# Optimization experiments

Measured on AMD Instinct MI355X. Metric: run time of the kernel, lower is better.

Reference implementation:

```python
import jax, jax.numpy as jnp
import numpy as np

B = 256      # batch
ZD = 128     # z_dim
HIN = 128    # H_inputs
H = 512      # hidden
HT = 32      # H_t
N = 16384    # num nodes
RW = 16      # rw_len
TEMP = 1.0
P_DROP = 0.2
EPS_C = 0.1  # constraints epsilon


def setup_inputs() -> dict:
    key = jax.random.key(0)
    ks = jax.random.split(key, 20)
    def w(k, shape, fan):
        return (jax.random.normal(k, shape, jnp.float32) / np.float32(np.sqrt(fan)))
    z = lambda n: jnp.zeros((n,), jnp.float32)
    u = jax.random.uniform(ks[14], (RW, B, N), jnp.float32)
    return {
        "latent": jax.random.normal(ks[0], (B, ZD + 1), jnp.float32),
        "inputs0": jnp.zeros((B, HIN), jnp.float32),
        "Wc": w(ks[1], (ZD, ZD + 1), ZD + 1), "bc": z(ZD),
        "Ws": w(ks[2], (H, ZD), ZD), "bs": z(H),
        "Wh": w(ks[3], (H, H), H), "bh": z(H),
        "Wcc": w(ks[4], (H, H), H), "bcc": z(H),
        "W_ih": w(ks[5], (4 * H, HIN), HIN), "b_ih": z(4 * H),
        "W_hh": w(ks[6], (4 * H, H), H), "b_hh": z(4 * H),
        "W_up": w(ks[7], (N, H), H), "b_up": z(N),
        "W_down": w(ks[8], (HIN, N), N),
        "Wt_down": w(ks[9], (HT, H), H), "bt_down": z(HT),
        "Wt_pred": w(ks[10], (1, HT), HT),
        "Wt_up": w(ks[11], (HT, 1), 1), "bt_up": z(HT),
        "W_vt": w(ks[12], (HIN, HIN + HT), HIN + HT),
        "W_prob": w(ks[13], (1, HIN), HIN),
        # pre-sampled Gumbel noise per step (torch.rand -> gumbel)
        "gumbel": -jnp.log(-jnp.log(u + 1e-20) + 1e-20),
        # uniforms for dropout masks in TimeDecoder (forced train mode)
        "drop_u": jax.random.uniform(ks[15], (RW, B, HT), jnp.float32),
    }


def reference(latent, inputs0, Wc, bc, Ws, bs, Wh, bh, Wcc, bcc,
              W_ih, b_ih, W_hh, b_hh, W_up, b_up, W_down,
              Wt_down, bt_down, Wt_pred, Wt_up, bt_up, W_vt, W_prob,
              gumbel, drop_u):
    # induced=True path: compress latent, init (h, c)
    lat = jnp.tanh(latent @ Wc.T + bc)               # [B, ZD]
    s = jnp.tanh(lat @ Ws.T + bs)                    # [B, H]
    h0 = jnp.tanh(s @ Wh.T + bh)
    c0 = jnp.tanh(s @ Wcc.T + bcc)
    keep = 1.0 - P_DROP

    def step(carry, xs):
        x, h, c, last_t = carry
        g, du = xs
        # torch LSTMCell: gate order i, f, g, o
        gates = x @ W_ih.T + b_ih + h @ W_hh.T + b_hh  # [B, 4H]
        i, f, gg, o = jnp.split(gates, 4, axis=1)
        c2 = jax.nn.sigmoid(f) * c + jax.nn.sigmoid(i) * jnp.tanh(gg)
        h2 = jax.nn.sigmoid(o) * jnp.tanh(c2)
        # node logits + gumbel-softmax sample
        p = h2 @ W_up.T + b_up                         # [B, N]
        v = jax.nn.softmax((p + g) / TEMP, axis=1)
        Hg = v @ W_down.T                              # [B, HIN]
        # TimeDecoder (dropout always in train mode)
        td = jnp.tanh(h2 @ Wt_down.T + bt_down)        # [B, HT]
        td = td * (du < keep).astype(td.dtype) / keep
        t = jnp.minimum(td @ Wt_pred.T, 1.0)           # [B, 1]
        # constraints(t, last_t)
        mn = jnp.min(t)
        t = jnp.where(mn < EPS_C, t - mn, t)
        mx = jnp.max(t)
        t = jnp.where(mx > 1.0, t / mx, t)
        t = jnp.clip(t, last_t, 1.0)
        Ht = t @ Wt_up.T + bt_up                       # [B, HT]
        x2 = jnp.concatenate([Hg, Ht], axis=1) @ W_vt.T  # [B, HIN]
        return (x2, h2, c2, t), (v, t)

    last_t0 = jnp.zeros((latent.shape[0], 1), latent.dtype)
    (xf, _, _, _), (rw, ts) = jax.lax.scan(step, (inputs0, h0, c0, last_t0), (gumbel, drop_u))
    rw = jnp.transpose(rw, (1, 0, 2))   # [B, RW, N]
    ts = jnp.transpose(ts, (1, 0, 2))   # [B, RW, 1]
    prob = xf @ W_prob.T                # [B, 1]
    return rw, ts, prob
```

## Files before the change

### kernel.cpp

```cpp
#include <hip/hip_runtime.h>

typedef float  __attribute__((ext_vector_type(4))) f32x4;
typedef int    __attribute__((ext_vector_type(4))) i32x4;
typedef unsigned short u16;
typedef unsigned long long u64;

#define B    256
#define H    512
#define HIN  128
#define N    16384
#define RW   16
#define HT   32
#define KC2  672
#define RWN  262144
#define TS_OFF   67108864
#define PROB_OFF 67112960

__device__ __forceinline__ u16 f2bf(float f) {
  unsigned u = __builtin_bit_cast(unsigned, f);
  u += 0x7FFFu + ((u >> 16) & 1u);
  return (u16)(u >> 16);
}
__device__ __forceinline__ float bf2f(u16 v) {
  return __builtin_bit_cast(float, ((unsigned)v) << 16);
}
__device__ __forceinline__ float sigm(float x) { return 1.0f / (1.0f + expf(-x)); }

__device__ __forceinline__ void mfma(f32x4& d, i32x4 a, i32x4 b) {
  asm volatile("v_mfma_f32_16x16x32_bf16 %0, %1, %2, %0" : "+v"(d) : "v"(a), "v"(b));
}
__device__ __forceinline__ void mfma_n(f32x4& d, i32x4 a, i32x4 b) {
  asm volatile("s_nop 1\n\tv_mfma_f32_16x16x32_bf16 %0, %1, %2, %0" : "+v"(d) : "v"(a), "v"(b));
}
__device__ __forceinline__ void fence_acc(f32x4& v) {
  asm volatile("s_nop 7\n\ts_nop 7" : "+v"(v));
}

__global__ __launch_bounds__(256) void k_prep(
    const float* __restrict__ W_up, const float* __restrict__ W_down,
    const float* __restrict__ W_hh, const float* __restrict__ Wt_down,
    const float* __restrict__ b_ih, const float* __restrict__ b_hh,
    const float* __restrict__ Wh, const float* __restrict__ Wcc,
    const float* __restrict__ W_ih, const float* __restrict__ W_vt,
    const float* __restrict__ inputs0, const float* __restrict__ W_prob,
    u16* __restrict__ Wup_b, u16* __restrict__ Wdn_b, u16* __restrict__ Wfull,
    u16* __restrict__ Wtd_b, u16* __restrict__ Whc_b,
    float* __restrict__ bcomb, float* __restrict__ tstep, float* __restrict__ rowLs,
    float* __restrict__ g0add, float* __restrict__ wpc)
{
  const int idx0 = blockIdx.x * 256 + threadIdx.x;
  const int stride = gridDim.x * 256;
  for (int i = idx0; i < N * H; i += stride) Wup_b[i] = f2bf(W_up[i]);
  for (int i = idx0; i < HIN * N; i += stride) Wdn_b[i] = f2bf(W_down[i]);
  for (int i = idx0; i < 4 * H * H; i += stride) {
    int j = i >> 9, k = i & 511;
    Wfull[j * KC2 + 160 + k] = f2bf(W_hh[i]);
  }
  for (int i = idx0; i < HT * H; i += stride) Wtd_b[i] = f2bf(Wt_down[i]);
  for (int i = idx0; i < 2 * H * H; i += stride) {
    int j = i >> 9, k = i & 511;
    Whc_b[i] = f2bf(j < H ? Wh[j * H + k] : Wcc[(j - H) * H + k]);
  }
  for (int i = idx0; i < 4 * H; i += stride) bcomb[i] = b_ih[i] + b_hh[i];
  for (int i = idx0; i < B; i += stride) tstep[i] = 0.0f;
  for (int i = idx0; i < 16 * B; i += stride) rowLs[i] = 0.0f;
  for (int i = idx0; i < 2048 * 160; i += stride) {
    int j = i / 160, m = i - j * 160;
    float a = 0.0f;
    for (int c = 0; c < HIN; ++c) a += W_ih[j * HIN + c] * W_vt[c * 160 + m];
    Wfull[j * KC2 + m] = f2bf(a);
  }
  for (int i = idx0; i < 256 * 2048; i += stride) {
    int b = i >> 11, j = i & 2047;
    float a = 0.0f;
    for (int k = 0; k < HIN; ++k) a += inputs0[b * HIN + k] * W_ih[j * HIN + k];
    g0add[i] = a;
  }
  for (int i = idx0; i < 160; i += stride) {
    float a = 0.0f;
    for (int k = 0; k < HIN; ++k) a += W_prob[k] * W_vt[k * 160 + i];
    wpc[i] = a;
  }
}

__global__ __launch_bounds__(256) void k_lat(
    const float* __restrict__ latent, const float* __restrict__ Wc,
    const float* __restrict__ bc, float* __restrict__ latbuf)
{
  int idx = blockIdx.x * 256 + threadIdx.x;
  int b = idx >> 7, i = idx & 127;
  float acc = bc[i];
  for (int k = 0; k < 129; ++k) acc += latent[b * 129 + k] * Wc[i * 129 + k];
  latbuf[idx] = tanhf(acc);
}

__global__ __launch_bounds__(256) void k_sinit(
    const float* __restrict__ latbuf, const float* __restrict__ Ws,
    const float* __restrict__ bs, u16* __restrict__ sinit_b)
{
  int idx = blockIdx.x * 256 + threadIdx.x;
  int b = idx >> 9, j = idx & 511;
  float acc = bs[j];
  for (int k = 0; k < HIN; ++k) acc += latbuf[b * HIN + k] * Ws[j * HIN + k];
  sinit_b[idx] = f2bf(tanhf(acc));
}

__global__ __launch_bounds__(256) void k_h0c0m(
    const u16* __restrict__ sinit_b, const u16* __restrict__ Whc_b,
    const float* __restrict__ bh, const float* __restrict__ bcc,
    float* __restrict__ cbuf, u16* __restrict__ h0out)
{
  const int rb = blockIdx.x >> 6, cb = blockIdx.x & 63;
  const int wave = threadIdx.x >> 6, lane = threadIdx.x & 63;
  const int lr = lane & 15, lk = lane >> 4;
  const int m0 = rb * 16, col0 = cb * 16;
  const u16* ab = sinit_b + (m0 + lr) * H + wave * 128 + 8 * lk;
  const u16* bb = Whc_b + (col0 + lr) * H + wave * 128 + 8 * lk;
  f32x4 acc[2] = {};
  mfma_n(acc[0], *(const i32x4*)(ab),      *(const i32x4*)(bb));
  mfma_n(acc[1], *(const i32x4*)(ab + 32), *(const i32x4*)(bb + 32));
  mfma(acc[0], *(const i32x4*)(ab + 64), *(const i32x4*)(bb + 64));
  mfma(acc[1], *(const i32x4*)(ab + 96), *(const i32x4*)(bb + 96));
  fence_acc(acc[0]); fence_acc(acc[1]);
  __shared__ float q[4][16][17];
  #pragma unroll
  for (int rr = 0; rr < 4; ++rr)
    q[wave][4 * lk + rr][lr] = acc[0][rr] + acc[1][rr];
  __syncthreads();
  const int r2 = threadIdx.x >> 4, jj = threadIdx.x & 15;
  float s = q[0][r2][jj] + q[1][r2][jj] + q[2][r2][jj] + q[3][r2][jj];
  int col = col0 + jj;
  if (col < H) h0out[(m0 + r2) * H + col] = f2bf(tanhf(s + bh[col]));
  else         cbuf[(m0 + r2) * H + col - H] = tanhf(s + bcc[col - H]);
}

__global__ __launch_bounds__(256) void k_lstm2(
    const u16* __restrict__ hprev, u16* __restrict__ hcur,
    const u16* __restrict__ Wfull, const float* __restrict__ bcomb,
    float* __restrict__ cbuf, const float* __restrict__ g0,
    const float* __restrict__ HgXprev, float* __restrict__ HgXcur,
    const float* __restrict__ rowLs, const float* __restrict__ t0buf,
    float* __restrict__ tstep, const float* __restrict__ Wt_up,
    const float* __restrict__ bt_up, float* __restrict__ out, int r)
{
  const int blk = blockIdx.x, tid = threadIdx.x;
  const int wave = tid >> 6, lane = tid & 63;
  const int lr = lane & 15, lk = lane >> 4;
  const int rb = blk & 15, cb = blk >> 4;
  const int m0 = rb * 16, j0 = cb * 16;
  const float* rowLprev = rowLs + (r - 1) * B;

  __shared__ u16 aT[16][168];
  __shared__ float q[4][16][17];
  __shared__ float redS[8];
  __shared__ float tl[256];

  HgXcur[blk * 512 + tid] = 0.0f;
  HgXcur[blk * 512 + 256 + tid] = 0.0f;

  float tv = 0.0f;
  if (r > 0) {
    tv = t0buf[tid];
    float v = tv;
    #pragma unroll
    for (int off = 1; off < 64; off <<= 1) v = fminf(v, __shfl_xor(v, off));
    if (lane == 0) redS[wave] = v;
  }
  __syncthreads();
  if (r > 0) {
    float mn = fminf(fminf(redS[0], redS[1]), fminf(redS[2], redS[3]));
    if (mn < 0.1f) tv -= mn;
    float v = tv;
    #pragma unroll
    for (int off = 1; off < 64; off <<= 1) v = fmaxf(v, __shfl_xor(v, off));
    if (lane == 0) redS[4 + wave] = v;
  }
  __syncthreads();
  if (r > 0) {
    float mx = fmaxf(fmaxf(redS[4], redS[5]), fmaxf(redS[6], redS[7]));
    if (mx > 1.0f) tv /= mx;
    tv = fminf(fmaxf(tv, tstep[(r - 1) * B + tid]), 1.0f);
    if (blk == 0) {
      tstep[r * B + tid] = tv;
      out[TS_OFF + tid * RW + (r - 1)] = tv;
    }
  }
  tl[tid] = tv;

  {
    const int row = tid >> 4, c8 = (tid & 15) * 8;
    if (r > 0) {
      const float* hp = HgXprev + (size_t)(m0 + row) * HIN + c8;
      f32x4 A0 = {}, A1 = {};
      #pragma unroll
      for (int x = 0; x < 8; ++x) {
        A0 += *(const f32x4*)(hp + (size_t)x * (B * HIN));
        A1 += *(const f32x4*)(hp + (size_t)x * (B * HIN) + 4);
      }
      float R = 1.0f / rowLprev[m0 + row];
      aT[row][c8 + 0] = f2bf(A0[0] * R); aT[row][c8 + 1] = f2bf(A0[1] * R);
      aT[row][c8 + 2] = f2bf(A0[2] * R); aT[row][c8 + 3] = f2bf(A0[3] * R);
      aT[row][c8 + 4] = f2bf(A1[0] * R); aT[row][c8 + 5] = f2bf(A1[1] * R);
      aT[row][c8 + 6] = f2bf(A1[2] * R); aT[row][c8 + 7] = f2bf(A1[3] * R);
    } else {
      #pragma unroll
      for (int e = 0; e < 8; ++e) aT[row][c8 + e] = 0;
    }
  }
  __syncthreads();

  for (int i2 = tid; i2 < 512; i2 += 256) {
    int row = i2 >> 5, j = i2 & 31;
    aT[row][128 + j] = (r > 0) ? f2bf(tl[m0 + row] * Wt_up[j] + bt_up[j]) : (u16)0;
  }
  __syncthreads();

  const int gcol = wave * H + j0 + lr;
  f32x4 acc[2] = {};
  const u16* brow = Wfull + (size_t)gcol * KC2 + 8 * lk;
  const u16* aL   = &aT[lr][8 * lk];
  const u16* arow = hprev + (m0 + lr) * H + 8 * lk;
  mfma_n(acc[0], *(const i32x4*)(aL),       *(const i32x4*)(brow));
  mfma_n(acc[1], *(const i32x4*)(aL + 32),  *(const i32x4*)(brow + 32));
  mfma(acc[0], *(const i32x4*)(aL + 64),  *(const i32x4*)(brow + 64));
  mfma(acc[1], *(const i32x4*)(aL + 96),  *(const i32x4*)(brow + 96));
  mfma(acc[0], *(const i32x4*)(aL + 128), *(const i32x4*)(brow + 128));
  #pragma unroll 4
  for (int i = 5; i < 21; ++i) {
    int kk = i * 32;
    mfma(acc[i & 1], *(const i32x4*)(arow + kk - 160), *(const i32x4*)(brow + kk));
  }
  fence_acc(acc[0]); fence_acc(acc[1]);
  float bias = bcomb[gcol];
  #pragma unroll
  for (int rr = 0; rr < 4; ++rr)
    q[wave][4 * lk + rr][lr] = acc[0][rr] + acc[1][rr] + bias;
  __syncthreads();
  const int r2 = tid >> 4, jj = tid & 15;
  const int b = m0 + r2, j = j0 + jj;
  float gi = q[0][r2][jj], gf = q[1][r2][jj], gg = q[2][r2][jj], go = q[3][r2][jj];
  if (r == 0) {
    const float* gp = g0 + b * 2048 + j;
    gi += gp[0]; gf += gp[512]; gg += gp[1024]; go += gp[1536];
  }
  float c  = cbuf[b * H + j];
  float c2 = sigm(gf) * c + sigm(gi) * tanhf(gg);
  float h2 = sigm(go) * tanhf(c2);
  cbuf[b * H + j] = c2;
  hcur[b * H + j] = f2bf(h2);
}

__global__ __launch_bounds__(256) void k_pgemm2(
    const u16* __restrict__ hb, const u16* __restrict__ Wup,
    const float* __restrict__ b_up, const float* __restrict__ gum,
    u16* __restrict__ eb, const u16* __restrict__ ebp,
    float* __restrict__ rowL, const float* __restrict__ rowLs,
    float* __restrict__ HgX, const u16* __restrict__ Wdn,
    const u16* __restrict__ Wtd, const float* __restrict__ bt_down,
    const float* __restrict__ Wt_pred, const float* __restrict__ du,
    float* __restrict__ t0, float* __restrict__ out, int r)
{
  const int blk = blockIdx.x;
  const int rb = blk >> 7, cb = blk & 127;
  const int wave = threadIdx.x >> 6, lane = threadIdx.x & 63;
  const int lr = lane & 15, lk = lane >> 4;
  const int m0 = rb * 32;
  const int n0 = cb * 128 + wave * 32;

  float gv[2][4][2], bup0 = b_up[n0 + lr], bup1 = b_up[n0 + 16 + lr];
  #pragma unroll
  for (int mi = 0; mi < 2; ++mi)
    #pragma unroll
    for (int rr = 0; rr < 4; ++rr) {
      int row = m0 + 16 * mi + 4 * lk + rr;
      gv[mi][rr][0] = gum[(size_t)row * N + n0 + lr];
      gv[mi][rr][1] = gum[(size_t)row * N + n0 + 16 + lr];
    }

  if (r > 0) {
    const float* rowLprev = rowLs + (r - 1) * B;
    #pragma unroll
    for (int uu = 0; uu < 4; ++uu) {
      int flat = (blk * 1024 + uu * 256 + (int)threadIdx.x) * 4;
      int row = flat >> 14;
      float Rv = 1.0f / rowLprev[row];
      u64 ev = *(const u64*)(ebp + flat);
      f32x4 o;
      o[0] = bf2f((u16)ev) * Rv;
      o[1] = bf2f((u16)(ev >> 16)) * Rv;
      o[2] = bf2f((u16)(ev >> 32)) * Rv;
      o[3] = bf2f((u16)(ev >> 48)) * Rv;
      *(f32x4*)(out + (size_t)row * RWN + (size_t)(r - 1) * N + (flat & (N - 1))) = o;
    }
  }

  f32x4 acc[2][2] = {};
  const u16* a0 = hb + (m0 + lr) * H + 8 * lk;
  const u16* a1 = a0 + 16 * H;
  const u16* b0 = Wup + (size_t)(n0 + lr) * H + 8 * lk;
  const u16* b1 = b0 + 16 * H;
  {
    i32x4 af0 = *(const i32x4*)(a0);
    i32x4 af1 = *(const i32x4*)(a1);
    i32x4 bf0 = *(const i32x4*)(b0);
    i32x4 bf1 = *(const i32x4*)(b1);
    mfma_n(acc[0][0], af0, bf0); mfma_n(acc[0][1], af0, bf1);
    mfma_n(acc[1][0], af1, bf0); mfma_n(acc[1][1], af1, bf1);
  }
  #pragma unroll 3
  for (int kk = 32; kk < H; kk += 32) {
    i32x4 af0 = *(const i32x4*)(a0 + kk);
    i32x4 af1 = *(const i32x4*)(a1 + kk);
    i32x4 bf0 = *(const i32x4*)(b0 + kk);
    i32x4 bf1 = *(const i32x4*)(b1 + kk);
    mfma(acc[0][0], af0, bf0); mfma(acc[0][1], af0, bf1);
    mfma(acc[1][0], af1, bf0); mfma(acc[1][1], af1, bf1);
  }
  #pragma unroll
  for (int mi = 0; mi < 2; ++mi) { fence_acc(acc[mi][0]); fence_acc(acc[mi][1]); }

  __shared__ u16 eLb[32][136];
  __shared__ float sL[4][32];
  #pragma unroll
  for (int mi = 0; mi < 2; ++mi)
    #pragma unroll
    for (int rr = 0; rr < 4; ++rr) {
      int rl = 16 * mi + 4 * lk + rr;
      int row = m0 + rl;
      u16* sp = eb + (size_t)row * N + n0 + lr;
      float v0 = acc[mi][0][rr] + bup0 + gv[mi][rr][0];
      float v1 = acc[mi][1][rr] + bup1 + gv[mi][rr][1];
      float e0 = expf(fminf(v0, 80.0f));
      float e1 = expf(fminf(v1, 80.0f));
      u16 p0 = f2bf(e0), p1 = f2bf(e1);
      sp[0] = p0; sp[16] = p1;
      eLb[rl][wave * 32 + lr] = p0;
      eLb[rl][wave * 32 + 16 + lr] = p1;
      float par = e0 + e1;
      #pragma unroll
      for (int off = 1; off < 16; off <<= 1) par += __shfl_xor(par, off);
      if (lr == 0) sL[wave][rl] = par;
    }
  __syncthreads();
  if (threadIdx.x < 32)
    atomicAdd(rowL + m0 + threadIdx.x,
              sL[0][threadIdx.x] + sL[1][threadIdx.x] + sL[2][threadIdx.x] + sL[3][threadIdx.x]);

  const int nb = cb * 128;
  float* hgs = HgX + (size_t)(blk & 7) * (B * HIN);
  f32x4 acc2[2][2] = {};
  #pragma unroll
  for (int kk2 = 0; kk2 < 4; ++kk2) {
    i32x4 af0 = *(const i32x4*)(&eLb[lr][kk2 * 32 + 8 * lk]);
    i32x4 af1 = *(const i32x4*)(&eLb[16 + lr][kk2 * 32 + 8 * lk]);
    i32x4 bf0 = *(const i32x4*)(Wdn + (size_t)(wave * 32 + lr) * N + nb + kk2 * 32 + 8 * lk);
    i32x4 bf1 = *(const i32x4*)(Wdn + (size_t)(wave * 32 + 16 + lr) * N + nb + kk2 * 32 + 8 * lk);
    mfma(acc2[0][0], af0, bf0); mfma(acc2[0][1], af0, bf1);
    mfma(acc2[1][0], af1, bf0); mfma(acc2[1][1], af1, bf1);
  }
  #pragma unroll
  for (int mi2 = 0; mi2 < 2; ++mi2) { fence_acc(acc2[mi2][0]); fence_acc(acc2[mi2][1]); }
  #pragma unroll
  for (int mi2 = 0; mi2 < 2; ++mi2)
    #pragma unroll
    for (int ni = 0; ni < 2; ++ni)
      #pragma unroll
      for (int rr = 0; rr < 4; ++rr)
        atomicAdd(hgs + (m0 + 16 * mi2 + 4 * lk + rr) * HIN + wave * 32 + 16 * ni + lr,
                  acc2[mi2][ni][rr]);

  if (cb == 0 && wave < 2) {
    f32x4 acc3[2] = {};
    const u16* at = hb + (m0 + wave * 16 + lr) * H + 8 * lk;
    {
      i32x4 af = *(const i32x4*)(at);
      mfma_n(acc3[0], af, *(const i32x4*)(Wtd + lr * H + 8 * lk));
      mfma_n(acc3[1], af, *(const i32x4*)(Wtd + (16 + lr) * H + 8 * lk));
    }
    for (int kk = 32; kk < H; kk += 32) {
      i32x4 af = *(const i32x4*)(at + kk);
      mfma(acc3[0], af, *(const i32x4*)(Wtd + lr * H + kk + 8 * lk));
      mfma(acc3[1], af, *(const i32x4*)(Wtd + (16 + lr) * H + kk + 8 * lk));
    }
    fence_acc(acc3[0]); fence_acc(acc3[1]);
    float wp0 = Wt_pred[lr],  wp1 = Wt_pred[16 + lr];
    float bt0 = bt_down[lr],  bt1 = bt_down[16 + lr];
    #pragma unroll
    for (int rr = 0; rr < 4; ++rr) {
      int row = m0 + wave * 16 + 4 * lk + rr;
      float td0 = tanhf(acc3[0][rr] + bt0);
      float td1 = tanhf(acc3[1][rr] + bt1);
      td0 = (du[row * HT + lr]      < 0.8f) ? td0 * 1.25f : 0.0f;
      td1 = (du[row * HT + 16 + lr] < 0.8f) ? td1 * 1.25f : 0.0f;
      float part = td0 * wp0 + td1 * wp1;
      #pragma unroll
      for (int off = 1; off < 16; off <<= 1) part += __shfl_xor(part, off);
      if (lr == 0) t0[row] = fminf(part, 1.0f);
    }
  }
}

__global__ __launch_bounds__(256) void k_tail(
    float* __restrict__ out, const u16* __restrict__ eb15,
    const float* __restrict__ rowLs, const float* __restrict__ t0buf,
    float* __restrict__ tstep, const float* __restrict__ HgX15,
    const float* __restrict__ Wt_up, const float* __restrict__ bt_up,
    const float* __restrict__ wpc)
{
  const int blk = blockIdx.x, tid = threadIdx.x;
  const float* rowL15 = rowLs + 15 * B;
  if (blk < 1024) {
    #pragma unroll
    for (int uu = 0; uu < 4; ++uu) {
      int flat = (blk * 1024 + uu * 256 + tid) * 4;
      int row = flat >> 14;
      float Rv = 1.0f / rowL15[row];
      u64 ev = *(const u64*)(eb15 + flat);
      f32x4 o;
      o[0] = bf2f((u16)ev) * Rv;
      o[1] = bf2f((u16)(ev >> 16)) * Rv;
      o[2] = bf2f((u16)(ev >> 32)) * Rv;
      o[3] = bf2f((u16)(ev >> 48)) * Rv;
      *(f32x4*)(out + (size_t)row * RWN + (size_t)15 * N + (flat & (N - 1))) = o;
    }
  }
  if (blk == 0 || blk == 1024) {
    const int wave = tid >> 6, lane = tid & 63;
    __shared__ float redS[8];
    float tv = t0buf[tid];
    float v = tv;
    #pragma unroll
    for (int off = 1; off < 64; off <<= 1) v = fminf(v, __shfl_xor(v, off));
    if (lane == 0) redS[wave] = v;
    __syncthreads();
    float mn = fminf(fminf(redS[0], redS[1]), fminf(redS[2], redS[3]));
    if (mn < 0.1f) tv -= mn;
    v = tv;
    #pragma unroll
    for (int off = 1; off < 64; off <<= 1) v = fmaxf(v, __shfl_xor(v, off));
    if (lane == 0) redS[4 + wave] = v;
    __syncthreads();
    float mx = fmaxf(fmaxf(redS[4], redS[5]), fmaxf(redS[6], redS[7]));
    if (mx > 1.0f) tv /= mx;
    tv = fminf(fmaxf(tv, tstep[15 * B + tid]), 1.0f);
    if (blk == 0) out[TS_OFF + tid * RW + 15] = tv;
    else {
      float R = 1.0f / rowL15[tid];
      float acc = 0.0f;
      for (int m = 0; m < HIN; ++m) {
        float hg = 0.0f;
        #pragma unroll
        for (int x = 0; x < 8; ++x) hg += HgX15[(size_t)x * (B * HIN) + tid * HIN + m];
        acc += hg * R * wpc[m];
      }
      for (int j = 0; j < HT; ++j) acc += (tv * Wt_up[j] + bt_up[j]) * wpc[HIN + j];
      out[PROB_OFF + tid] = acc;
    }
  }
}

extern "C" void kernel_launch(void* const* d_in, const int* in_sizes, int n_in,
                              void* d_out, int out_size, void* d_ws, size_t ws_size,
                              hipStream_t stream) {
  (void)in_sizes; (void)n_in; (void)out_size; (void)ws_size;
  const float* latent  = (const float*)d_in[0];
  const float* inputs0 = (const float*)d_in[1];
  const float* Wc      = (const float*)d_in[2];
  const float* bc      = (const float*)d_in[3];
  const float* Ws      = (const float*)d_in[4];
  const float* bs      = (const float*)d_in[5];
  const float* Wh      = (const float*)d_in[6];
  const float* bh      = (const float*)d_in[7];
  const float* Wcc     = (const float*)d_in[8];
  const float* bcc     = (const float*)d_in[9];
  const float* W_ih    = (const float*)d_in[10];
  const float* b_ih    = (const float*)d_in[11];
  const float* W_hh    = (const float*)d_in[12];
  const float* b_hh    = (const float*)d_in[13];
  const float* W_up    = (const float*)d_in[14];
  const float* b_up    = (const float*)d_in[15];
  const float* W_down  = (const float*)d_in[16];
  const float* Wt_down = (const float*)d_in[17];
  const float* bt_down = (const float*)d_in[18];
  const float* Wt_pred = (const float*)d_in[19];
  const float* Wt_up   = (const float*)d_in[20];
  const float* bt_up   = (const float*)d_in[21];
  const float* W_vt    = (const float*)d_in[22];
  const float* W_prob  = (const float*)d_in[23];
  const float* gumbel  = (const float*)d_in[24];
  const float* drop_u  = (const float*)d_in[25];
  float* out = (float*)d_out;

  char* p = (char*)d_ws;
  auto alloc = [&](size_t bytes) { char* r = p; p += (bytes + 255) & ~(size_t)255; return r; };
  u16*   Wup_b  = (u16*)  alloc((size_t)N * H * 2);
  u16*   Wdn_b  = (u16*)  alloc((size_t)HIN * N * 2);
  u16*   Wfull_b= (u16*)  alloc((size_t)4 * H * KC2 * 2);
  u16*   Wtd_b  = (u16*)  alloc((size_t)HT * H * 2);
  u16*   Whc_b  = (u16*)  alloc((size_t)2 * H * H * 2);
  float* bcomb  = (float*)alloc(4 * H * 4);
  u16*   hbuf0  = (u16*)  alloc((size_t)B * H * 2);
  u16*   hbuf1  = (u16*)  alloc((size_t)B * H * 2);
  float* cbuf   = (float*)alloc((size_t)B * H * 4);
  u16*   sinit_b= (u16*)  alloc((size_t)B * H * 2);
  float* latbuf = (float*)alloc((size_t)B * HIN * 4);
  float* rowLs  = (float*)alloc((size_t)16 * B * 4);
  float* t0buf  = (float*)alloc(B * 4);
  float* tstep  = (float*)alloc((size_t)17 * B * 4);
  float* HgX0   = (float*)alloc((size_t)8 * B * HIN * 4);
  float* HgX1   = (float*)alloc((size_t)8 * B * HIN * 4);
  float* g0add  = (float*)alloc((size_t)B * 4 * H * 4);
  float* wpc    = (float*)alloc(160 * 4);
  u16*   ebuf0  = (u16*)  alloc((size_t)B * N * 2);
  u16*   ebuf1  = (u16*)  alloc((size_t)B * N * 2);

  k_prep<<<2048, 256, 0, stream>>>(W_up, W_down, W_hh, Wt_down, b_ih, b_hh, Wh, Wcc,
                                   W_ih, W_vt, inputs0, W_prob,
                                   Wup_b, Wdn_b, Wfull_b, Wtd_b, Whc_b, bcomb,
                                   tstep, rowLs, g0add, wpc);
  k_lat  <<<128, 256, 0, stream>>>(latent, Wc, bc, latbuf);
  k_sinit<<<512, 256, 0, stream>>>(latbuf, Ws, bs, sinit_b);
  k_h0c0m<<<1024, 256, 0, stream>>>(sinit_b, Whc_b, bh, bcc, cbuf, hbuf1);

  for (int r = 0; r < 16; ++r) {
    u16* hprev = (r & 1) ? hbuf0 : hbuf1;
    u16* hcur  = (r & 1) ? hbuf1 : hbuf0;
    u16* eb    = (r & 1) ? ebuf1 : ebuf0;
    u16* ebp   = (r & 1) ? ebuf0 : ebuf1;
    float* HgXc = (r & 1) ? HgX1 : HgX0;
    float* HgXp = (r & 1) ? HgX0 : HgX1;
    k_lstm2<<<512, 256, 0, stream>>>(hprev, hcur, Wfull_b, bcomb, cbuf, g0add,
                                     HgXp, HgXc, rowLs, t0buf, tstep,
                                     Wt_up, bt_up, out, r);
    k_pgemm2<<<1024, 256, 0, stream>>>(hcur, Wup_b, b_up, gumbel + (size_t)r * B * N,
                                       eb, ebp, rowLs + r * B, rowLs, HgXc, Wdn_b,
                                       Wtd_b, bt_down, Wt_pred,
                                       drop_u + (size_t)r * B * HT, t0buf, out, r);
  }
  k_tail<<<1025, 256, 0, stream>>>(out, ebuf1, rowLs, t0buf, tstep, HgX1,
                                   Wt_up, bt_up, wpc);
}
```

Measured before the change: 1.354 ms.

## Move softmax output writeback into LSTM kernel and shrink projection row tile

The normalization and fp32 store of the previous step's random-walk probabilities moves from the node-projection kernel into the LSTM kernel, which has a lighter workload. The projection kernel's row tile drops from 32 to 16 rows, doubling its grid to 2048 blocks. The eight partial Hg accumulation slices are replaced by one B×HIN buffer, so readers no longer sum slices. The costs are that each W_up tile is now reused across fewer rows, and more blocks issue atomics onto the same addresses, raising contention.

Measured after the change: 1.541 ms. +13.8%, slower.

```diff
diff --git a/kernel.cpp b/kernel.cpp
--- a/kernel.cpp
+++ b/kernel.cpp
@@ -138,10 +138,11 @@
     const u16* __restrict__ hprev, u16* __restrict__ hcur,
     const u16* __restrict__ Wfull, const float* __restrict__ bcomb,
     float* __restrict__ cbuf, const float* __restrict__ g0,
-    const float* __restrict__ HgXprev, float* __restrict__ HgXcur,
+    const float* __restrict__ HgfPrev, float* __restrict__ HgfNext,
     const float* __restrict__ rowLs, const float* __restrict__ t0buf,
     float* __restrict__ tstep, const float* __restrict__ Wt_up,
-    const float* __restrict__ bt_up, float* __restrict__ out, int r)
+    const float* __restrict__ bt_up, float* __restrict__ out,
+    const u16* __restrict__ ebp, int r)
 {
   const int blk = blockIdx.x, tid = threadIdx.x;
   const int wave = tid >> 6, lane = tid & 63;
@@ -155,8 +156,7 @@
   __shared__ float redS[8];
   __shared__ float tl[256];
 
-  HgXcur[blk * 512 + tid] = 0.0f;
-  HgXcur[blk * 512 + 256 + tid] = 0.0f;
+  if (blk < 128) HgfNext[blk * 256 + tid] = 0.0f;
 
   float tv = 0.0f;
   if (r > 0) {
@@ -190,18 +190,14 @@
   {
     const int row = tid >> 4, c8 = (tid & 15) * 8;
     if (r > 0) {
-      const float* hp = HgXprev + (size_t)(m0 + row) * HIN + c8;
-      f32x4 A0 = {}, A1 = {};
-      #pragma unroll
-      for (int x = 0; x < 8; ++x) {
-        A0 += *(const f32x4*)(hp + (size_t)x * (B * HIN));
-        A1 += *(const f32x4*)(hp + (size_t)x * (B * HIN) + 4);
-      }
+      const float* hp = HgfPrev + (m0 + row) * HIN + c8;
+      f32x4 x0 = *(const f32x4*)hp;
+      f32x4 x1 = *(const f32x4*)(hp + 4);
       float R = 1.0f / rowLprev[m0 + row];
-      aT[row][c8 + 0] = f2bf(A0[0] * R); aT[row][c8 + 1] = f2bf(A0[1] * R);
-      aT[row][c8 + 2] = f2bf(A0[2] * R); aT[row][c8 + 3] = f2bf(A0[3] * R);
-      aT[row][c8 + 4] = f2bf(A1[0] * R); aT[row][c8 + 5] = f2bf(A1[1] * R);
-      aT[row][c8 + 6] = f2bf(A1[2] * R); aT[row][c8 + 7] = f2bf(A1[3] * R);
+      aT[row][c8 + 0] = f2bf(x0[0] * R); aT[row][c8 + 1] = f2bf(x0[1] * R);
+      aT[row][c8 + 2] = f2bf(x0[2] * R); aT[row][c8 + 3] = f2bf(x0[3] * R);
+      aT[row][c8 + 4] = f2bf(x1[0] * R); aT[row][c8 + 5] = f2bf(x1[1] * R);
+      aT[row][c8 + 6] = f2bf(x1[2] * R); aT[row][c8 + 7] = f2bf(x1[3] * R);
     } else {
       #pragma unroll
       for (int e = 0; e < 8; ++e) aT[row][c8 + e] = 0;
@@ -212,6 +208,22 @@
   for (int i2 = tid; i2 < 512; i2 += 256) {
     int row = i2 >> 5, j = i2 & 31;
     aT[row][128 + j] = (r > 0) ? f2bf(tl[m0 + row] * Wt_up[j] + bt_up[j]) : (u16)0;
+  }
+
+  if (r > 0) {
+    #pragma unroll
+    for (int uu = 0; uu < 8; ++uu) {
+      int flat = (blk * 2048 + uu * 256 + tid) * 4;
+      int row = flat >> 14;
+      float Rv = 1.0f / rowLprev[row];
+      u64 ev = *(const u64*)(ebp + flat);
+      f32x4 o;
+      o[0] = bf2f((u16)ev) * Rv;
+      o[1] = bf2f((u16)(ev >> 16)) * Rv;
+      o[2] = bf2f((u16)(ev >> 32)) * Rv;
+      o[3] = bf2f((u16)(ev >> 48)) * Rv;
+      *(f32x4*)(out + (size_t)row * RWN + (size_t)(r - 1) * N + (flat & (N - 1))) = o;
+    }
   }
   __syncthreads();
 
@@ -253,125 +265,89 @@
 __global__ __launch_bounds__(256) void k_pgemm2(
     const u16* __restrict__ hb, const u16* __restrict__ Wup,
     const float* __restrict__ b_up, const float* __restrict__ gum,
-    u16* __restrict__ eb, const u16* __restrict__ ebp,
-    float* __restrict__ rowL, const float* __restrict__ rowLs,
-    float* __restrict__ HgX, const u16* __restrict__ Wdn,
+    u16* __restrict__ eb, float* __restrict__ rowL,
+    float* __restrict__ HgfAcc, const u16* __restrict__ Wdn,
     const u16* __restrict__ Wtd, const float* __restrict__ bt_down,
     const float* __restrict__ Wt_pred, const float* __restrict__ du,
-    float* __restrict__ t0, float* __restrict__ out, int r)
-{
-  const int blk = blockIdx.x;
-  const int rb = blk >> 7, cb = blk & 127;
+    float* __restrict__ t0)
+{
+  const int rb = blockIdx.x >> 7, cb = blockIdx.x & 127;
   const int wave = threadIdx.x >> 6, lane = threadIdx.x & 63;
   const int lr = lane & 15, lk = lane >> 4;
-  const int m0 = rb * 32;
+  const int m0 = rb * 16;
   const int n0 = cb * 128 + wave * 32;
 
-  float gv[2][4][2], bup0 = b_up[n0 + lr], bup1 = b_up[n0 + 16 + lr];
+  float gv[4][2], bup0 = b_up[n0 + lr], bup1 = b_up[n0 + 16 + lr];
   #pragma unroll
-  for (int mi = 0; mi < 2; ++mi)
-    #pragma unroll
-    for (int rr = 0; rr < 4; ++rr) {
-      int row = m0 + 16 * mi + 4 * lk + rr;
-      gv[mi][rr][0] = gum[(size_t)row * N + n0 + lr];
-      gv[mi][rr][1] = gum[(size_t)row * N + n0 + 16 + lr];
-    }
-
-  if (r > 0) {
-    const float* rowLprev = rowLs + (r - 1) * B;
-    #pragma unroll
-    for (int uu = 0; uu < 4; ++uu) {
-      int flat = (blk * 1024 + uu * 256 + (int)threadIdx.x) * 4;
-      int row = flat >> 14;
-      float Rv = 1.0f / rowLprev[row];
-      u64 ev = *(const u64*)(ebp + flat);
-      f32x4 o;
-      o[0] = bf2f((u16)ev) * Rv;
-      o[1] = bf2f((u16)(ev >> 16)) * Rv;
-      o[2] = bf2f((u16)(ev >> 32)) * Rv;
-      o[3] = bf2f((u16)(ev >> 48)) * Rv;
-      *(f32x4*)(out + (size_t)row * RWN + (size_t)(r - 1) * N + (flat & (N - 1))) = o;
-    }
-  }
-
-  f32x4 acc[2][2] = {};
+  for (int rr = 0; rr < 4; ++rr) {
+    int row = m0 + 4 * lk + rr;
+    gv[rr][0] = gum[(size_t)row * N + n0 + lr];
+    gv[rr][1] = gum[(size_t)row * N + n0 + 16 + lr];
+  }
+
+  f32x4 acc[2] = {};
   const u16* a0 = hb + (m0 + lr) * H + 8 * lk;
-  const u16* a1 = a0 + 16 * H;
   const u16* b0 = Wup + (size_t)(n0 + lr) * H + 8 * lk;
   const u16* b1 = b0 + 16 * H;
   {
     i32x4 af0 = *(const i32x4*)(a0);
-    i32x4 af1 = *(const i32x4*)(a1);
-    i32x4 bf0 = *(const i32x4*)(b0);
-    i32x4 bf1 = *(const i32x4*)(b1);
-    mfma_n(acc[0][0], af0, bf0); mfma_n(acc[0][1], af0, bf1);
-    mfma_n(acc[1][0], af1, bf0); mfma_n(acc[1][1], af1, bf1);
+    mfma_n(acc[0], af0, *(const i32x4*)(b0));
+    mfma_n(acc[1], af0, *(const i32x4*)(b1));
   }
   #pragma unroll 3
   for (int kk = 32; kk < H; kk += 32) {
     i32x4 af0 = *(const i32x4*)(a0 + kk);
-    i32x4 af1 = *(const i32x4*)(a1 + kk);
-    i32x4 bf0 = *(const i32x4*)(b0 + kk);
-    i32x4 bf1 = *(const i32x4*)(b1 + kk);
-    mfma(acc[0][0], af0, bf0); mfma(acc[0][1], af0, bf1);
-    mfma(acc[1][0], af1, bf0); mfma(acc[1][1], af1, bf1);
-  }
+    mfma(acc[0], af0, *(const i32x4*)(b0 + kk));
+    mfma(acc[1], af0, *(const i32x4*)(b1 + kk));
+  }
+  fence_acc(acc[0]); fence_acc(acc[1]);
+
+  __shared__ u16 eLb[16][168];
+  __shared__ float sL[4][16];
   #pragma unroll
-  for (int mi = 0; mi < 2; ++mi) { fence_acc(acc[mi][0]); fence_acc(acc[mi][1]); }
-
-  __shared__ u16 eLb[32][136];
-  __shared__ float sL[4][32];
-  #pragma unroll
-  for (int mi = 0; mi < 2; ++mi)
-    #pragma unroll
-    for (int rr = 0; rr < 4; ++rr) {
-      int rl = 16 * mi + 4 * lk + rr;
-      int row = m0 + rl;
-      u16* sp = eb + (size_t)row * N + n0 + lr;
-      float v0 = acc[mi][0][rr] + bup0 + gv[mi][rr][0];
-      float v1 = acc[mi][1][rr] + bup1 + gv[mi][rr][1];
-      float e0 = expf(fminf(v0, 80.0f));
-      float e1 = expf(fminf(v1, 80.0f));
-      u16 p0 = f2bf(e0), p1 = f2bf(e1);
-      sp[0] = p0; sp[16] = p1;
-      eLb[rl][wave * 32 + lr] = p0;
-      eLb[rl][wave * 32 + 16 + lr] = p1;
-      float par = e0 + e1;
-      #pragma unroll
-      for (int off = 1; off < 16; off <<= 1) par += __shfl_xor(par, off);
-      if (lr == 0) sL[wave][rl] = par;
-    }
-  __syncthreads();
-  if (threadIdx.x < 32)
+  for (int rr = 0; rr < 4; ++rr) {
+    int rl = 4 * lk + rr;
+    int row = m0 + rl;
+    u16* sp = eb + (size_t)row * N + n0 + lr;
+    float v0 = acc[0][rr] + bup0 + gv[rr][0];
+    float v1 = acc[1][rr] + bup1 + gv[rr][1];
+    float e0 = expf(fminf(v0, 80.0f));
+    float e1 = expf(fminf(v1, 80.0f));
+    u16 p0 = f2bf(e0), p1 = f2bf(e1);
+    sp[0] = p0; sp[16] = p1;
+    eLb[rl][wave * 32 + lr] = p0;
+    eLb[rl][wave * 32 + 16 + lr] = p1;
+    float par = e0 + e1;
+    #pragma unroll
+    for (int off = 1; off < 16; off <<= 1) par += __shfl_xor(par, off);
+    if (lr == 0) sL[wave][rl] = par;
+  }
+  __syncthreads();
+  if (threadIdx.x < 16)
     atomicAdd(rowL + m0 + threadIdx.x,
               sL[0][threadIdx.x] + sL[1][threadIdx.x] + sL[2][threadIdx.x] + sL[3][threadIdx.x]);
 
   const int nb = cb * 128;
-  float* hgs = HgX + (size_t)(blk & 7) * (B * HIN);
-  f32x4 acc2[2][2] = {};
+  f32x4 acc2[2] = {};
   #pragma unroll
   for (int kk2 = 0; kk2 < 4; ++kk2) {
     i32x4 af0 = *(const i32x4*)(&eLb[lr][kk2 * 32 + 8 * lk]);
-    i32x4 af1 = *(const i32x4*)(&eLb[16 + lr][kk2 * 32 + 8 * lk]);
     i32x4 bf0 = *(const i32x4*)(Wdn + (size_t)(wave * 32 + lr) * N + nb + kk2 * 32 + 8 * lk);
     i32x4 bf1 = *(const i32x4*)(Wdn + (size_t)(wave * 32 + 16 + lr) * N + nb + kk2 * 32 + 8 * lk);
-    mfma(acc2[0][0], af0, bf0); mfma(acc2[0][1], af0, bf1);
-    mfma(acc2[1][0], af1, bf0); mfma(acc2[1][1], af1, bf1);
-  }
+    mfma(acc2[0], af0, bf0);
+    mfma(acc2[1], af0, bf1);
+  }
+  fence_acc(acc2[0]); fence_acc(acc2[1]);
   #pragma unroll
-  for (int mi2 = 0; mi2 < 2; ++mi2) { fence_acc(acc2[mi2][0]); fence_acc(acc2[mi2][1]); }
-  #pragma unroll
-  for (int mi2 = 0; mi2 < 2; ++mi2)
-    #pragma unroll
-    for (int ni = 0; ni < 2; ++ni)
-      #pragma unroll
-      for (int rr = 0; rr < 4; ++rr)
-        atomicAdd(hgs + (m0 + 16 * mi2 + 4 * lk + rr) * HIN + wave * 32 + 16 * ni + lr,
-                  acc2[mi2][ni][rr]);
-
-  if (cb == 0 && wave < 2) {
+  for (int ni = 0; ni < 2; ++ni)
+    #pragma unroll
+    for (int rr = 0; rr < 4; ++rr)
+      atomicAdd(HgfAcc + (m0 + 4 * lk + rr) * HIN + wave * 32 + 16 * ni + lr,
+                acc2[ni][rr]);
+
+  if (cb == 0 && wave == 0) {
     f32x4 acc3[2] = {};
-    const u16* at = hb + (m0 + wave * 16 + lr) * H + 8 * lk;
+    const u16* at = hb + (m0 + lr) * H + 8 * lk;
     {
       i32x4 af = *(const i32x4*)(at);
       mfma_n(acc3[0], af, *(const i32x4*)(Wtd + lr * H + 8 * lk));
@@ -387,7 +363,7 @@
     float bt0 = bt_down[lr],  bt1 = bt_down[16 + lr];
     #pragma unroll
     for (int rr = 0; rr < 4; ++rr) {
-      int row = m0 + wave * 16 + 4 * lk + rr;
+      int row = m0 + 4 * lk + rr;
       float td0 = tanhf(acc3[0][rr] + bt0);
       float td1 = tanhf(acc3[1][rr] + bt1);
       td0 = (du[row * HT + lr]      < 0.8f) ? td0 * 1.25f : 0.0f;
@@ -403,7 +379,7 @@
 __global__ __launch_bounds__(256) void k_tail(
     float* __restrict__ out, const u16* __restrict__ eb15,
     const float* __restrict__ rowLs, const float* __restrict__ t0buf,
-    float* __restrict__ tstep, const float* __restrict__ HgX15,
+    float* __restrict__ tstep, const float* __restrict__ Hgf15,
     const float* __restrict__ Wt_up, const float* __restrict__ bt_up,
     const float* __restrict__ wpc)
 {
@@ -447,12 +423,7 @@
     else {
       float R = 1.0f / rowL15[tid];
       float acc = 0.0f;
-      for (int m = 0; m < HIN; ++m) {
-        float hg = 0.0f;
-        #pragma unroll
-        for (int x = 0; x < 8; ++x) hg += HgX15[(size_t)x * (B * HIN) + tid * HIN + m];
-        acc += hg * R * wpc[m];
-      }
+      for (int m = 0; m < HIN; ++m) acc += Hgf15[tid * HIN + m] * R * wpc[m];
       for (int j = 0; j < HT; ++j) acc += (tv * Wt_up[j] + bt_up[j]) * wpc[HIN + j];
       out[PROB_OFF + tid] = acc;
     }
@@ -507,8 +478,8 @@
   float* rowLs  = (float*)alloc((size_t)16 * B * 4);
   float* t0buf  = (float*)alloc(B * 4);
   float* tstep  = (float*)alloc((size_t)17 * B * 4);
-  float* HgX0   = (float*)alloc((size_t)8 * B * HIN * 4);
-  float* HgX1   = (float*)alloc((size_t)8 * B * HIN * 4);
+  float* Hgf2_0 = (float*)alloc((size_t)B * HIN * 4);
+  float* Hgf2_1 = (float*)alloc((size_t)B * HIN * 4);
   float* g0add  = (float*)alloc((size_t)B * 4 * H * 4);
   float* wpc    = (float*)alloc(160 * 4);
   u16*   ebuf0  = (u16*)  alloc((size_t)B * N * 2);
@@ -527,16 +498,16 @@
     u16* hcur  = (r & 1) ? hbuf1 : hbuf0;
     u16* eb    = (r & 1) ? ebuf1 : ebuf0;
     u16* ebp   = (r & 1) ? ebuf0 : ebuf1;
-    float* HgXc = (r & 1) ? HgX1 : HgX0;
-    float* HgXp = (r & 1) ? HgX0 : HgX1;
+    float* HgfCur  = (r & 1) ? Hgf2_1 : Hgf2_0;
+    float* HgfPrev = (r & 1) ? Hgf2_0 : Hgf2_1;
     k_lstm2<<<512, 256, 0, stream>>>(hprev, hcur, Wfull_b, bcomb, cbuf, g0add,
-                                     HgXp, HgXc, rowLs, t0buf, tstep,
-                                     Wt_up, bt_up, out, r);
-    k_pgemm2<<<1024, 256, 0, stream>>>(hcur, Wup_b, b_up, gumbel + (size_t)r * B * N,
-                                       eb, ebp, rowLs + r * B, rowLs, HgXc, Wdn_b,
+                                     HgfPrev, HgfCur, rowLs, t0buf, tstep,
+                                     Wt_up, bt_up, out, ebp, r);
+    k_pgemm2<<<2048, 256, 0, stream>>>(hcur, Wup_b, b_up, gumbel + (size_t)r * B * N,
+                                       eb, rowLs + r * B, HgfCur, Wdn_b,
                                        Wtd_b, bt_down, Wt_pred,
-                                       drop_u + (size_t)r * B * HT, t0buf, out, r);
-  }
-  k_tail<<<1025, 256, 0, stream>>>(out, ebuf1, rowLs, t0buf, tstep, HgX1,
+                                       drop_u + (size_t)r * B * HT, t0buf);
+  }
+  k_tail<<<1025, 256, 0, stream>>>(out, ebuf1, rowLs, t0buf, tstep, Hgf2_1,
                                    Wt_up, bt_up, wpc);
 }
```
